# Kernel tuning notes

Measured on AMD Instinct MI355X. Metric: run time of the kernel, lower is better.

The kernel has to match this reference:

```python
import jax, jax.numpy as jnp
import numpy as np

B, S, D, H = 2, 2048, 1024, 16
DH = D // H  # 64


def setup_inputs() -> dict:
    key = jax.random.key(0)
    ks = jax.random.split(key, 6)
    scale = 1.0 / np.sqrt(D)
    x = jax.random.normal(ks[0], (B, S, D), dtype=jnp.float32)
    Wq = jax.random.normal(ks[1], (D, D), dtype=jnp.float32) * scale
    Wk = jax.random.normal(ks[2], (D, D), dtype=jnp.float32) * scale
    Wv = jax.random.normal(ks[3], (D, D), dtype=jnp.float32) * scale
    Wo = jax.random.normal(ks[4], (D, D), dtype=jnp.float32) * scale
    zeros = jnp.zeros((D,), dtype=jnp.float32)
    return {"x": x, "Wq": Wq, "bq": zeros, "Wk": Wk, "bk": zeros,
            "Wv": Wv, "bv": zeros, "Wo": Wo, "bo": zeros}


def reference(x, Wq, bq, Wk, bk, Wv, bv, Wo, bo):
    # x: [B, S, D]
    def split_heads(t):
        # [B, S, D] -> [B, H, S, DH]
        return t.reshape(B, S, H, DH).transpose(0, 2, 1, 3)

    q = split_heads(x @ Wq + bq)
    k = split_heads(x @ Wk + bk)
    v = split_heads(x @ Wv + bv)

    scores = jnp.einsum('bhqd,bhkd->bhqk', q, k) / jnp.sqrt(jnp.float32(DH))
    weights = jax.nn.softmax(scores, axis=-1)          # [B, H, S, S]
    o = jnp.einsum('bhqk,bhkd->bhqd', weights, v)       # [B, H, S, DH]
    o = o.transpose(0, 2, 1, 3).reshape(B, S, D)        # merge heads
    return o @ Wo + bo
```

## Files before the change

kernel.cpp:

```cpp
#include <hip/hip_runtime.h>
#include <hip/hip_bf16.h>

#define DEV __device__ __forceinline__

typedef short bf16x8 __attribute__((ext_vector_type(8)));
typedef float f32x4 __attribute__((ext_vector_type(4)));
typedef unsigned int u32;

constexpr int BB = 2, SS = 2048, DD = 1024, HH = 16, DHD = 64;
constexpr int MM = BB * SS;
#define QSC 0.1803368801111f

#if __has_builtin(__builtin_amdgcn_exp2f)
#define EXP2(x) __builtin_amdgcn_exp2f(x)
#else
#define EXP2(x) exp2f(x)
#endif

DEV unsigned short f2bf(float f) {
    union { float f; unsigned int u; } v; v.f = f;
    return (unsigned short)((v.u + 0x8000u) >> 16);
}
#if __has_builtin(__builtin_amdgcn_perm)
DEV u32 pk2bf(float a, float b) {
    union { float f; u32 u; } ua, ub; ua.f = a; ub.f = b;
    return __builtin_amdgcn_perm(ub.u + 0x8000u, ua.u + 0x8000u, 0x07060302u);
}
#else
DEV u32 pk2bf(float a, float b) {
    union { float f; u32 u; } ua, ub; ua.f = a; ub.f = b;
    return ((ua.u + 0x8000u) >> 16) | ((ub.u + 0x8000u) & 0xffff0000u);
}
#endif

DEV bf16x8 ld_bf16x8(const unsigned short* p) { return *(const bf16x8*)p; }

DEV void gl16(const unsigned short* g, unsigned short* l) {
    __builtin_amdgcn_global_load_lds(
        (const __attribute__((address_space(1))) u32*)g,
        (__attribute__((address_space(3))) u32*)l, 16, 0, 0);
}

__global__ void prep(const float* __restrict__ x, unsigned short* __restrict__ xb,
                     const float* __restrict__ W0, const float* __restrict__ W1,
                     const float* __restrict__ W2, const float* __restrict__ W3,
                     unsigned short* __restrict__ WtBase) {
    __shared__ float tile[32][33];
    int blk = blockIdx.x;
    if (blk < 4096) {
        int i = blk * 256 + threadIdx.x;
        float4 v = ((const float4*)x)[i];
        uint2 o;
        o.x = pk2bf(v.x, v.y);
        o.y = pk2bf(v.z, v.w);
        ((uint2*)xb)[i] = o;
        return;
    }
    blk -= 4096;
    int wsel = blk >> 10;
    const float* W = (wsel == 0) ? W0 : (wsel == 1) ? W1 : (wsel == 2) ? W2 : W3;
    unsigned short* Wt = WtBase + (size_t)wsel * DD * DD;
    int t = blk & 1023;
    int n0 = (t & 31) * 32, k0 = (t >> 5) * 32;
    int tx = threadIdx.x & 31, ty = threadIdx.x >> 5;
    #pragma unroll
    for (int i = 0; i < 4; ++i)
        tile[ty + 8 * i][tx] = W[(size_t)(k0 + ty + 8 * i) * DD + n0 + tx];
    __syncthreads();
    #pragma unroll
    for (int i = 0; i < 4; ++i)
        Wt[(size_t)(n0 + ty + 8 * i) * DD + k0 + tx] = f2bf(tile[tx][ty + 8 * i]);
}

__global__ __launch_bounds__(256) void qkv_gemm(
    const unsigned short* __restrict__ xb,
    const unsigned short* __restrict__ WtBase,
    const float* __restrict__ bq, const float* __restrict__ bk, const float* __restrict__ bv,
    unsigned short* __restrict__ Qb, unsigned short* __restrict__ Kb, unsigned short* __restrict__ Vt)
{
    __shared__ __align__(16) unsigned short Ald[2][128 * 32];
    __shared__ __align__(16) unsigned short Bld[2][128 * 32];

    const int z = blockIdx.z;
    const unsigned short* Wt = WtBase + (size_t)z * DD * DD;
    const float* bias = (z == 0) ? bq : (z == 1) ? bk : bv;

    const int m0g = blockIdx.y * 128;
    const int n0g = blockIdx.x * 128;
    const int wave = threadIdx.x >> 6, lane = threadIdx.x & 63;
    const int quad = lane >> 4, lcol = lane & 15;
    const int mb = (wave & 1) * 64, nb = (wave >> 1) * 64;

    f32x4 acc[4][4];
    #pragma unroll
    for (int i = 0; i < 4; ++i)
        #pragma unroll
        for (int j = 0; j < 4; ++j) acc[i][j] = (f32x4){0.f, 0.f, 0.f, 0.f};

    auto stage = [&](int ks, int bf) {
        #pragma unroll
        for (int i = 0; i < 4; ++i) {
            int j = wave * 4 + i;
            if (j < 8) {
                int bi = j * 64 + lane;
                int row = bi >> 2, p = (bi & 3) ^ (row & 3);
                gl16(xb + (size_t)(m0g + row) * DD + ks + p * 8, &Ald[bf][j * 512]);
            } else {
                int jj = j - 8;
                int bi = jj * 64 + lane;
                int row = bi >> 2, p = (bi & 3) ^ (row & 3);
                gl16(Wt + (size_t)(n0g + row) * DD + ks + p * 8, &Bld[bf][jj * 512]);
            }
        }
    };

    stage(0, 0);
    __syncthreads();

    for (int kk = 0; kk < 32; ++kk) {
        int bf = kk & 1;
        if (kk + 1 < 32) stage((kk + 1) * 32, (kk + 1) & 1);
        bf16x8 af[4], bfr[4];
        #pragma unroll
        for (int mt = 0; mt < 4; ++mt) {
            int row = mb + mt * 16 + lcol;
            af[mt] = ld_bf16x8(&Ald[bf][(row * 4 + (quad ^ (row & 3))) * 8]);
        }
        #pragma unroll
        for (int nt = 0; nt < 4; ++nt) {
            int row = nb + nt * 16 + lcol;
            bfr[nt] = ld_bf16x8(&Bld[bf][(row * 4 + (quad ^ (row & 3))) * 8]);
        }
        if (z < 2) {
            #pragma unroll
            for (int mt = 0; mt < 4; ++mt)
                #pragma unroll
                for (int nt = 0; nt < 4; ++nt)
                    acc[mt][nt] = __builtin_amdgcn_mfma_f32_16x16x32_bf16(bfr[nt], af[mt], acc[mt][nt], 0, 0, 0);
        } else {
            #pragma unroll
            for (int mt = 0; mt < 4; ++mt)
                #pragma unroll
                for (int nt = 0; nt < 4; ++nt)
                    acc[mt][nt] = __builtin_amdgcn_mfma_f32_16x16x32_bf16(af[mt], bfr[nt], acc[mt][nt], 0, 0, 0);
        }
        __syncthreads();
    }

    if (z < 2) {
        unsigned short* dst = (z == 0) ? Qb : Kb;
        const float sc = (z == 0) ? QSC : 1.0f;
        #pragma unroll
        for (int mt = 0; mt < 4; ++mt)
            #pragma unroll
            for (int nt = 0; nt < 4; ++nt) {
                int m = m0g + mb + mt * 16 + lcol;
                int nbt = n0g + nb + nt * 16 + quad * 4;
                int b = m >> 11, s = m & (SS - 1);
                int h = nbt >> 6, dh0 = nbt & 63;
                float4 bv4 = *(const float4*)&bias[nbt];
                uint2 o;
                o.x = pk2bf((acc[mt][nt][0] + bv4.x) * sc, (acc[mt][nt][1] + bv4.y) * sc);
                o.y = pk2bf((acc[mt][nt][2] + bv4.z) * sc, (acc[mt][nt][3] + bv4.w) * sc);
                *(uint2*)&dst[(((size_t)b * HH + h) * SS + s) * DHD + dh0] = o;
            }
    } else {
        #pragma unroll
        for (int mt = 0; mt < 4; ++mt)
            #pragma unroll
            for (int nt = 0; nt < 4; ++nt) {
                int n = n0g + nb + nt * 16 + lcol;
                int mbt = m0g + mb + mt * 16 + quad * 4;
                int h = n >> 6, dh = n & 63;
                int b = mbt >> 11, s0 = mbt & (SS - 1);
                float bvv = bias[n];
                uint2 o;
                o.x = pk2bf(acc[mt][nt][0] + bvv, acc[mt][nt][1] + bvv);
                o.y = pk2bf(acc[mt][nt][2] + bvv, acc[mt][nt][3] + bvv);
                *(uint2*)&Vt[(((size_t)b * HH + h) * DHD + dh) * SS + s0] = o;
            }
    }
}

__global__ __launch_bounds__(512, 4) void attn(
    const unsigned short* __restrict__ Qb,
    const unsigned short* __restrict__ Kb,
    const unsigned short* __restrict__ Vt,
    unsigned short* __restrict__ Ob)
{
    __shared__ __align__(16) unsigned short Kld[2][64 * 64];
    __shared__ __align__(16) unsigned short Vld[2][64 * 64];
    __shared__ __align__(16) unsigned short tb[8][16 * 68];

    const int g = blockIdx.y * gridDim.x + blockIdx.x;
    const int bh = (g & 7) * 4 + ((g >> 3) & 3);
    const int qt = g >> 5;
    const int b = bh >> 4, h = bh & (HH - 1);
    const unsigned short* Qbh = Qb + (size_t)bh * SS * DHD;
    const unsigned short* Kbh = Kb + (size_t)bh * SS * DHD;
    const unsigned short* Vbh = Vt + (size_t)bh * DHD * SS;

    const int wave = threadIdx.x >> 6, lane = threadIdx.x & 63;
    const int quad = lane >> 4, lcol = lane & 15;
    const int rowbase = qt * 128 + wave * 16;

    bf16x8 qf0 = ld_bf16x8(Qbh + (size_t)(rowbase + lcol) * DHD + quad * 8);
    bf16x8 qf1 = ld_bf16x8(Qbh + (size_t)(rowbase + lcol) * DHD + 32 + quad * 8);

    auto stage = [&](int c, int bf) {
        int kb = c * 64;
        #pragma unroll
        for (int i = 0; i < 2; ++i) {
            int j = wave * 2 + i;
            if (j < 8) {
                int bi = j * 64 + lane;
                int r = bi >> 3, p = (bi & 7) ^ (r & 7);
                gl16(Kbh + (size_t)(kb + r) * DHD + p * 8, &Kld[bf][j * 512]);
            } else {
                int jj = j - 8;
                int bi = jj * 64 + lane;
                int dh = bi >> 3, p = (bi & 7) ^ (dh & 7);
                gl16(Vbh + (size_t)dh * SS + kb + p * 8, &Vld[bf][jj * 512]);
            }
        }
    };

    stage(0, 0);
    __syncthreads();

    float m0 = -1e30f;
    #pragma unroll
    for (int kt = 0; kt < 4; ++kt) {
        int r0 = kt * 16 + lcol;
        bf16x8 ka0 = ld_bf16x8(&Kld[0][(r0 * 8 + (quad ^ (r0 & 7))) * 8]);
        bf16x8 ka1 = ld_bf16x8(&Kld[0][(r0 * 8 + ((quad + 4) ^ (r0 & 7))) * 8]);
        f32x4 s = (f32x4){0.f, 0.f, 0.f, 0.f};
        s = __builtin_amdgcn_mfma_f32_16x16x32_bf16(ka0, qf0, s, 0, 0, 0);
        s = __builtin_amdgcn_mfma_f32_16x16x32_bf16(ka1, qf1, s, 0, 0, 0);
        #pragma unroll
        for (int r = 0; r < 4; ++r) m0 = fmaxf(m0, s[r]);
    }
    #pragma unroll
    for (int msk = 1; msk < 64; msk <<= 1) m0 = fmaxf(m0, __shfl_xor(m0, msk, 64));
    const f32x4 minit = (f32x4){-m0, -m0, -m0, -m0};

    f32x4 oacc[4];
    #pragma unroll
    for (int nt = 0; nt < 4; ++nt) oacc[nt] = (f32x4){0.f, 0.f, 0.f, 0.f};
    float ps = 0.f;

    for (int c = 0; c < 32; ++c) {
        int bf = c & 1;
        if (c + 1 < 32) stage(c + 1, (c + 1) & 1);

        #pragma unroll
        for (int kt = 0; kt < 4; ++kt) {
            int r0 = kt * 16 + lcol;
            bf16x8 ka0 = ld_bf16x8(&Kld[bf][(r0 * 8 + (quad ^ (r0 & 7))) * 8]);
            bf16x8 ka1 = ld_bf16x8(&Kld[bf][(r0 * 8 + ((quad + 4) ^ (r0 & 7))) * 8]);
            f32x4 s = minit;
            s = __builtin_amdgcn_mfma_f32_16x16x32_bf16(ka0, qf0, s, 0, 0, 0);
            s = __builtin_amdgcn_mfma_f32_16x16x32_bf16(ka1, qf1, s, 0, 0, 0);
            float e0 = EXP2(s[0]), e1 = EXP2(s[1]);
            float e2 = EXP2(s[2]), e3 = EXP2(s[3]);
            ps += (e0 + e1) + (e2 + e3);
            *(uint2*)&tb[wave][lcol * 68 + kt * 16 + quad * 4] =
                make_uint2(pk2bf(e0, e1), pk2bf(e2, e3));
        }

        #pragma unroll
        for (int kf2 = 0; kf2 < 2; ++kf2) {
            bf16x8 pa = *(const bf16x8*)&tb[wave][lcol * 68 + kf2 * 32 + quad * 8];
            #pragma unroll
            for (int nt = 0; nt < 4; ++nt) {
                int dh = nt * 16 + lcol;
                bf16x8 vb = ld_bf16x8(&Vld[bf][(dh * 8 + ((kf2 * 4 + quad) ^ (dh & 7))) * 8]);
                oacc[nt] = __builtin_amdgcn_mfma_f32_16x16x32_bf16(pa, vb, oacc[nt], 0, 0, 0);
            }
        }
        __syncthreads();
    }

    ps += __shfl_xor(ps, 16, 64);
    ps += __shfl_xor(ps, 32, 64);
    float inv = 1.0f / ps;
    #pragma unroll
    for (int r = 0; r < 4; ++r) {
        float iv = __shfl(inv, quad * 4 + r, 64);
        int srow = rowbase + quad * 4 + r;
        size_t base = (((size_t)b * SS + srow) * HH + h) * DHD;
        #pragma unroll
        for (int nt = 0; nt < 4; ++nt)
            Ob[base + nt * 16 + lcol] = f2bf(oacc[nt][r] * iv);
    }
}

__global__ __launch_bounds__(256) void out_gemm(
    const unsigned short* __restrict__ Ob,
    const unsigned short* __restrict__ Wto,
    const float* __restrict__ bo,
    float* __restrict__ out)
{
    __shared__ __align__(16) unsigned short Ald[2][64 * 32];
    __shared__ __align__(16) unsigned short Bld[2][128 * 32];

    const int m0g = blockIdx.y * 64;
    const int n0g = blockIdx.x * 128;
    const int wave = threadIdx.x >> 6, lane = threadIdx.x & 63;
    const int quad = lane >> 4, lcol = lane & 15;
    const int nb = wave * 32;

    f32x4 acc[4][2];
    #pragma unroll
    for (int i = 0; i < 4; ++i)
        #pragma unroll
        for (int j = 0; j < 2; ++j) acc[i][j] = (f32x4){0.f, 0.f, 0.f, 0.f};

    auto stage = [&](int ks, int bf) {
        #pragma unroll
        for (int i = 0; i < 3; ++i) {
            int j = wave * 3 + i;
            if (j < 4) {
                int bi = j * 64 + lane;
                int row = bi >> 2, p = (bi & 3) ^ (row & 3);
                gl16(Ob + (size_t)(m0g + row) * DD + ks + p * 8, &Ald[bf][j * 512]);
            } else {
                int jj = j - 4;
                int bi = jj * 64 + lane;
                int row = bi >> 2, p = (bi & 3) ^ (row & 3);
                gl16(Wto + (size_t)(n0g + row) * DD + ks + p * 8, &Bld[bf][jj * 512]);
            }
        }
    };

    stage(0, 0);
    __syncthreads();

    for (int kk = 0; kk < 32; ++kk) {
        int bf = kk & 1;
        if (kk + 1 < 32) stage((kk + 1) * 32, (kk + 1) & 1);
        bf16x8 af[4], bfr[2];
        #pragma unroll
        for (int mt = 0; mt < 4; ++mt) {
            int row = mt * 16 + lcol;
            af[mt] = ld_bf16x8(&Ald[bf][(row * 4 + (quad ^ (row & 3))) * 8]);
        }
        #pragma unroll
        for (int nt = 0; nt < 2; ++nt) {
            int row = nb + nt * 16 + lcol;
            bfr[nt] = ld_bf16x8(&Bld[bf][(row * 4 + (quad ^ (row & 3))) * 8]);
        }
        #pragma unroll
        for (int mt = 0; mt < 4; ++mt)
            #pragma unroll
            for (int nt = 0; nt < 2; ++nt)
                acc[mt][nt] = __builtin_amdgcn_mfma_f32_16x16x32_bf16(af[mt], bfr[nt], acc[mt][nt], 0, 0, 0);
        __syncthreads();
    }

    #pragma unroll
    for (int mt = 0; mt < 4; ++mt)
        #pragma unroll
        for (int nt = 0; nt < 2; ++nt) {
            int n = n0g + nb + nt * 16 + lcol;
            float bv_ = bo[n];
            #pragma unroll
            for (int r = 0; r < 4; ++r) {
                int m = m0g + mt * 16 + quad * 4 + r;
                out[(size_t)m * DD + n] = acc[mt][nt][r] + bv_;
            }
        }
}

extern "C" void kernel_launch(void* const* d_in, const int* in_sizes, int n_in,
                              void* d_out, int out_size, void* d_ws, size_t ws_size,
                              hipStream_t stream)
{
    const float* x  = (const float*)d_in[0];
    const float* Wq = (const float*)d_in[1];
    const float* bq = (const float*)d_in[2];
    const float* Wk = (const float*)d_in[3];
    const float* bk = (const float*)d_in[4];
    const float* Wv = (const float*)d_in[5];
    const float* bv = (const float*)d_in[6];
    const float* Wo = (const float*)d_in[7];
    const float* bo = (const float*)d_in[8];
    float* out = (float*)d_out;

    unsigned short* ws = (unsigned short*)d_ws;
    unsigned short* Wt  = ws;
    unsigned short* Wto = Wt + 3 * (size_t)DD * DD;
    unsigned short* Qb  = Wt + 4 * (size_t)DD * DD;
    unsigned short* Kb  = Qb + (size_t)MM * DD;
    unsigned short* Vt  = Kb + (size_t)MM * DD;
    unsigned short* xb  = Vt + (size_t)MM * DD;
    unsigned short* Ob  = xb;

    prep<<<8192, 256, 0, stream>>>(x, xb, Wq, Wk, Wv, Wo, Wt);

    qkv_gemm<<<dim3(DD / 128, MM / 128, 3), 256, 0, stream>>>(xb, Wt, bq, bk, bv, Qb, Kb, Vt);

    attn<<<dim3(16, 32), 512, 0, stream>>>(Qb, Kb, Vt, Ob);

    out_gemm<<<dim3(DD / 128, MM / 64), 256, 0, stream>>>(Ob, Wto, bo, out);
}
```

Before: 210.4 us.

## Process two query tiles per wave in attention to reuse K/V fragments

The attention kernel drops from 8 waves to 4 per block, and each wave now handles 32 query rows (two 16-row tiles) instead of 16. K and V fragments are loaded from LDS once per chunk into registers and reused for both tiles, roughly halving LDS read traffic per unit of MFMA work. This raises register pressure through the doubled accumulators and held fragments, and it gives fewer waves per block to hide latency. Staging work per wave also doubles.

Result: slower. 216.3 us (+2.8%).

```diff
diff --git a/kernel.cpp b/kernel.cpp
--- a/kernel.cpp
+++ b/kernel.cpp
@@ -182,7 +182,7 @@
     }
 }
 
-__global__ __launch_bounds__(512, 4) void attn(
+__global__ __launch_bounds__(256) void attn(
     const unsigned short* __restrict__ Qb,
     const unsigned short* __restrict__ Kb,
     const unsigned short* __restrict__ Vt,
@@ -190,7 +190,7 @@
 {
     __shared__ __align__(16) unsigned short Kld[2][64 * 64];
     __shared__ __align__(16) unsigned short Vld[2][64 * 64];
-    __shared__ __align__(16) unsigned short tb[8][16 * 68];
+    __shared__ __align__(16) unsigned short tb[4][16 * 68];
 
     const int g = blockIdx.y * gridDim.x + blockIdx.x;
     const int bh = (g & 7) * 4 + ((g >> 3) & 3);
@@ -202,16 +202,20 @@
 
     const int wave = threadIdx.x >> 6, lane = threadIdx.x & 63;
     const int quad = lane >> 4, lcol = lane & 15;
-    const int rowbase = qt * 128 + wave * 16;
-
-    bf16x8 qf0 = ld_bf16x8(Qbh + (size_t)(rowbase + lcol) * DHD + quad * 8);
-    bf16x8 qf1 = ld_bf16x8(Qbh + (size_t)(rowbase + lcol) * DHD + 32 + quad * 8);
+    const int rowbase = qt * 128 + wave * 32;
+
+    bf16x8 qf[2][2];
+    #pragma unroll
+    for (int mt = 0; mt < 2; ++mt)
+        #pragma unroll
+        for (int kf = 0; kf < 2; ++kf)
+            qf[mt][kf] = ld_bf16x8(Qbh + (size_t)(rowbase + mt * 16 + lcol) * DHD + kf * 32 + quad * 8);
 
     auto stage = [&](int c, int bf) {
         int kb = c * 64;
         #pragma unroll
-        for (int i = 0; i < 2; ++i) {
-            int j = wave * 2 + i;
+        for (int i = 0; i < 4; ++i) {
+            int j = wave * 4 + i;
             if (j < 8) {
                 int bi = j * 64 + lane;
                 int r = bi >> 3, p = (bi & 7) ^ (r & 7);
@@ -234,65 +238,87 @@
         int r0 = kt * 16 + lcol;
         bf16x8 ka0 = ld_bf16x8(&Kld[0][(r0 * 8 + (quad ^ (r0 & 7))) * 8]);
         bf16x8 ka1 = ld_bf16x8(&Kld[0][(r0 * 8 + ((quad + 4) ^ (r0 & 7))) * 8]);
-        f32x4 s = (f32x4){0.f, 0.f, 0.f, 0.f};
-        s = __builtin_amdgcn_mfma_f32_16x16x32_bf16(ka0, qf0, s, 0, 0, 0);
-        s = __builtin_amdgcn_mfma_f32_16x16x32_bf16(ka1, qf1, s, 0, 0, 0);
-        #pragma unroll
-        for (int r = 0; r < 4; ++r) m0 = fmaxf(m0, s[r]);
+        #pragma unroll
+        for (int mt = 0; mt < 2; ++mt) {
+            f32x4 s = (f32x4){0.f, 0.f, 0.f, 0.f};
+            s = __builtin_amdgcn_mfma_f32_16x16x32_bf16(ka0, qf[mt][0], s, 0, 0, 0);
+            s = __builtin_amdgcn_mfma_f32_16x16x32_bf16(ka1, qf[mt][1], s, 0, 0, 0);
+            #pragma unroll
+            for (int r = 0; r < 4; ++r) m0 = fmaxf(m0, s[r]);
+        }
     }
     #pragma unroll
     for (int msk = 1; msk < 64; msk <<= 1) m0 = fmaxf(m0, __shfl_xor(m0, msk, 64));
     const f32x4 minit = (f32x4){-m0, -m0, -m0, -m0};
 
-    f32x4 oacc[4];
-    #pragma unroll
-    for (int nt = 0; nt < 4; ++nt) oacc[nt] = (f32x4){0.f, 0.f, 0.f, 0.f};
-    float ps = 0.f;
+    f32x4 oacc[2][4];
+    #pragma unroll
+    for (int mt = 0; mt < 2; ++mt)
+        #pragma unroll
+        for (int nt = 0; nt < 4; ++nt) oacc[mt][nt] = (f32x4){0.f, 0.f, 0.f, 0.f};
+    float ps[2] = {0.f, 0.f};
 
     for (int c = 0; c < 32; ++c) {
         int bf = c & 1;
         if (c + 1 < 32) stage(c + 1, (c + 1) & 1);
 
+        bf16x8 ka[4][2];
         #pragma unroll
         for (int kt = 0; kt < 4; ++kt) {
             int r0 = kt * 16 + lcol;
-            bf16x8 ka0 = ld_bf16x8(&Kld[bf][(r0 * 8 + (quad ^ (r0 & 7))) * 8]);
-            bf16x8 ka1 = ld_bf16x8(&Kld[bf][(r0 * 8 + ((quad + 4) ^ (r0 & 7))) * 8]);
-            f32x4 s = minit;
-            s = __builtin_amdgcn_mfma_f32_16x16x32_bf16(ka0, qf0, s, 0, 0, 0);
-            s = __builtin_amdgcn_mfma_f32_16x16x32_bf16(ka1, qf1, s, 0, 0, 0);
-            float e0 = EXP2(s[0]), e1 = EXP2(s[1]);
-            float e2 = EXP2(s[2]), e3 = EXP2(s[3]);
-            ps += (e0 + e1) + (e2 + e3);
-            *(uint2*)&tb[wave][lcol * 68 + kt * 16 + quad * 4] =
-                make_uint2(pk2bf(e0, e1), pk2bf(e2, e3));
-        }
-
-        #pragma unroll
-        for (int kf2 = 0; kf2 < 2; ++kf2) {
-            bf16x8 pa = *(const bf16x8*)&tb[wave][lcol * 68 + kf2 * 32 + quad * 8];
+            ka[kt][0] = ld_bf16x8(&Kld[bf][(r0 * 8 + (quad ^ (r0 & 7))) * 8]);
+            ka[kt][1] = ld_bf16x8(&Kld[bf][(r0 * 8 + ((quad + 4) ^ (r0 & 7))) * 8]);
+        }
+        bf16x8 vb[2][4];
+        #pragma unroll
+        for (int kf2 = 0; kf2 < 2; ++kf2)
             #pragma unroll
             for (int nt = 0; nt < 4; ++nt) {
                 int dh = nt * 16 + lcol;
-                bf16x8 vb = ld_bf16x8(&Vld[bf][(dh * 8 + ((kf2 * 4 + quad) ^ (dh & 7))) * 8]);
-                oacc[nt] = __builtin_amdgcn_mfma_f32_16x16x32_bf16(pa, vb, oacc[nt], 0, 0, 0);
+                vb[kf2][nt] = ld_bf16x8(&Vld[bf][(dh * 8 + ((kf2 * 4 + quad) ^ (dh & 7))) * 8]);
+            }
+
+        #pragma unroll
+        for (int mt = 0; mt < 2; ++mt) {
+            #pragma unroll
+            for (int kt = 0; kt < 4; ++kt) {
+                f32x4 s = minit;
+                s = __builtin_amdgcn_mfma_f32_16x16x32_bf16(ka[kt][0], qf[mt][0], s, 0, 0, 0);
+                s = __builtin_amdgcn_mfma_f32_16x16x32_bf16(ka[kt][1], qf[mt][1], s, 0, 0, 0);
+                float e0 = EXP2(s[0]), e1 = EXP2(s[1]);
+                float e2 = EXP2(s[2]), e3 = EXP2(s[3]);
+                ps[mt] += (e0 + e1) + (e2 + e3);
+                *(uint2*)&tb[wave][lcol * 68 + kt * 16 + quad * 4] =
+                    make_uint2(pk2bf(e0, e1), pk2bf(e2, e3));
+            }
+            #pragma unroll
+            for (int kf2 = 0; kf2 < 2; ++kf2) {
+                bf16x8 pa = *(const bf16x8*)&tb[wave][lcol * 68 + kf2 * 32 + quad * 8];
+                #pragma unroll
+                for (int nt = 0; nt < 4; ++nt)
+                    oacc[mt][nt] = __builtin_amdgcn_mfma_f32_16x16x32_bf16(pa, vb[kf2][nt], oacc[mt][nt], 0, 0, 0);
             }
         }
         __syncthreads();
     }
 
-    ps += __shfl_xor(ps, 16, 64);
-    ps += __shfl_xor(ps, 32, 64);
-    float inv = 1.0f / ps;
-    #pragma unroll
-    for (int r = 0; r < 4; ++r) {
-        float iv = __shfl(inv, quad * 4 + r, 64);
-        int srow = rowbase + quad * 4 + r;
-        size_t base = (((size_t)b * SS + srow) * HH + h) * DHD;
-        #pragma unroll
-        for (int nt = 0; nt < 4; ++nt)
-            Ob[base + nt * 16 + lcol] = f2bf(oacc[nt][r] * iv);
-    }
+    #pragma unroll
+    for (int mt = 0; mt < 2; ++mt) {
+        ps[mt] += __shfl_xor(ps[mt], 16, 64);
+        ps[mt] += __shfl_xor(ps[mt], 32, 64);
+    }
+    float inv[2] = {1.0f / ps[0], 1.0f / ps[1]};
+    #pragma unroll
+    for (int mt = 0; mt < 2; ++mt)
+        #pragma unroll
+        for (int r = 0; r < 4; ++r) {
+            float iv = __shfl(inv[mt], quad * 4 + r, 64);
+            int srow = rowbase + mt * 16 + quad * 4 + r;
+            size_t base = (((size_t)b * SS + srow) * HH + h) * DHD;
+            #pragma unroll
+            for (int nt = 0; nt < 4; ++nt)
+                Ob[base + nt * 16 + lcol] = f2bf(oacc[mt][nt][r] * iv);
+        }
 }
 
 __global__ __launch_bounds__(256) void out_gemm(
@@ -400,7 +426,7 @@
 
     qkv_gemm<<<dim3(DD / 128, MM / 128, 3), 256, 0, stream>>>(xb, Wt, bq, bk, bv, Qb, Kb, Vt);
 
-    attn<<<dim3(16, 32), 512, 0, stream>>>(Qb, Kb, Vt, Ob);
+    attn<<<dim3(16, 32), 256, 0, stream>>>(Qb, Kb, Vt, Ob);
 
     out_gemm<<<dim3(DD / 128, MM / 64), 256, 0, stream>>>(Ob, Wto, bo, out);
 }
```

## Deepen out-projection K tile and swap MFMA operands for vectorized stores

Applied to the files above, without the earlier changes.

The out-projection GEMM now stages 64-wide K slices with an 8-way XOR swizzle, halving the number of loop iterations and barriers. It also swaps the MFMA operand roles so the weight tile is the A operand, transposing the accumulator layout so each lane holds four consecutive output columns. That allows float4 bias loads and float4 output stores in place of scalar stores. Shared memory per block doubles, which may reduce occupancy.

Measured after the change: 203.3 us. -3.4%, faster.

```diff
diff --git a/kernel.cpp b/kernel.cpp
--- a/kernel.cpp
+++ b/kernel.cpp
@@ -301,8 +301,8 @@
     const float* __restrict__ bo,
     float* __restrict__ out)
 {
-    __shared__ __align__(16) unsigned short Ald[2][64 * 32];
-    __shared__ __align__(16) unsigned short Bld[2][128 * 32];
+    __shared__ __align__(16) unsigned short Wld[2][128 * 64];
+    __shared__ __align__(16) unsigned short Old[2][64 * 64];
 
     const int m0g = blockIdx.y * 64;
     const int n0g = blockIdx.x * 128;
@@ -310,25 +310,25 @@
     const int quad = lane >> 4, lcol = lane & 15;
     const int nb = wave * 32;
 
-    f32x4 acc[4][2];
-    #pragma unroll
-    for (int i = 0; i < 4; ++i)
-        #pragma unroll
-        for (int j = 0; j < 2; ++j) acc[i][j] = (f32x4){0.f, 0.f, 0.f, 0.f};
+    f32x4 acc[2][4];
+    #pragma unroll
+    for (int i = 0; i < 2; ++i)
+        #pragma unroll
+        for (int j = 0; j < 4; ++j) acc[i][j] = (f32x4){0.f, 0.f, 0.f, 0.f};
 
     auto stage = [&](int ks, int bf) {
         #pragma unroll
-        for (int i = 0; i < 3; ++i) {
-            int j = wave * 3 + i;
-            if (j < 4) {
+        for (int i = 0; i < 6; ++i) {
+            int j = wave * 6 + i;
+            if (j < 16) {
                 int bi = j * 64 + lane;
-                int row = bi >> 2, p = (bi & 3) ^ (row & 3);
-                gl16(Ob + (size_t)(m0g + row) * DD + ks + p * 8, &Ald[bf][j * 512]);
+                int r = bi >> 3, p = (bi & 7) ^ (r & 7);
+                gl16(Wto + (size_t)(n0g + r) * DD + ks + p * 8, &Wld[bf][j * 512]);
             } else {
-                int jj = j - 4;
+                int jj = j - 16;
                 int bi = jj * 64 + lane;
-                int row = bi >> 2, p = (bi & 3) ^ (row & 3);
-                gl16(Wto + (size_t)(n0g + row) * DD + ks + p * 8, &Bld[bf][jj * 512]);
+                int r = bi >> 3, p = (bi & 7) ^ (r & 7);
+                gl16(Ob + (size_t)(m0g + r) * DD + ks + p * 8, &Old[bf][jj * 512]);
             }
         }
     };
@@ -336,40 +336,46 @@
     stage(0, 0);
     __syncthreads();
 
-    for (int kk = 0; kk < 32; ++kk) {
+    for (int kk = 0; kk < 16; ++kk) {
         int bf = kk & 1;
-        if (kk + 1 < 32) stage((kk + 1) * 32, (kk + 1) & 1);
-        bf16x8 af[4], bfr[2];
-        #pragma unroll
-        for (int mt = 0; mt < 4; ++mt) {
-            int row = mt * 16 + lcol;
-            af[mt] = ld_bf16x8(&Ald[bf][(row * 4 + (quad ^ (row & 3))) * 8]);
-        }
-        #pragma unroll
-        for (int nt = 0; nt < 2; ++nt) {
-            int row = nb + nt * 16 + lcol;
-            bfr[nt] = ld_bf16x8(&Bld[bf][(row * 4 + (quad ^ (row & 3))) * 8]);
-        }
-        #pragma unroll
-        for (int mt = 0; mt < 4; ++mt)
-            #pragma unroll
-            for (int nt = 0; nt < 2; ++nt)
-                acc[mt][nt] = __builtin_amdgcn_mfma_f32_16x16x32_bf16(af[mt], bfr[nt], acc[mt][nt], 0, 0, 0);
+        if (kk + 1 < 16) stage((kk + 1) * 64, (kk + 1) & 1);
+        #pragma unroll
+        for (int kh = 0; kh < 2; ++kh) {
+            bf16x8 wf[2], of[4];
+            #pragma unroll
+            for (int i = 0; i < 2; ++i) {
+                int row = nb + i * 16 + lcol;
+                wf[i] = ld_bf16x8(&Wld[bf][(row * 8 + ((kh * 4 + quad) ^ (row & 7))) * 8]);
+            }
+            #pragma unroll
+            for (int j = 0; j < 4; ++j) {
+                int row = j * 16 + lcol;
+                of[j] = ld_bf16x8(&Old[bf][(row * 8 + ((kh * 4 + quad) ^ (row & 7))) * 8]);
+            }
+            #pragma unroll
+            for (int i = 0; i < 2; ++i)
+                #pragma unroll
+                for (int j = 0; j < 4; ++j)
+                    acc[i][j] = __builtin_amdgcn_mfma_f32_16x16x32_bf16(wf[i], of[j], acc[i][j], 0, 0, 0);
+        }
         __syncthreads();
     }
 
     #pragma unroll
-    for (int mt = 0; mt < 4; ++mt)
-        #pragma unroll
-        for (int nt = 0; nt < 2; ++nt) {
-            int n = n0g + nb + nt * 16 + lcol;
-            float bv_ = bo[n];
-            #pragma unroll
-            for (int r = 0; r < 4; ++r) {
-                int m = m0g + mt * 16 + quad * 4 + r;
-                out[(size_t)m * DD + n] = acc[mt][nt][r] + bv_;
-            }
-        }
+    for (int i = 0; i < 2; ++i) {
+        int n4 = n0g + nb + i * 16 + quad * 4;
+        float4 bv4 = *(const float4*)&bo[n4];
+        #pragma unroll
+        for (int j = 0; j < 4; ++j) {
+            int token = m0g + j * 16 + lcol;
+            float4 o;
+            o.x = acc[i][j][0] + bv4.x;
+            o.y = acc[i][j][1] + bv4.y;
+            o.z = acc[i][j][2] + bv4.z;
+            o.w = acc[i][j][3] + bv4.w;
+            *(float4*)&out[(size_t)token * DD + n4] = o;
+        }
+    }
 }
 
 extern "C" void kernel_launch(void* const* d_in, const int* in_sizes, int n_in,
```
